# Performance work log

Hardware: AMD Instinct MI355X
Metric: run time of the kernel (lower is better)

## Reference

```python
import jax, jax.numpy as jnp
import numpy as np
import math

B, N, D, H = 2, 96, 64, 4  # batch, num_nodes, d_model, num_heads
DK = D // H


def setup_inputs() -> dict:
    key = jax.random.key(0)
    ks = jax.random.split(key, 11)
    s = 0.02
    return {
        "state": jax.random.normal(ks[0], (B, N * N, D), jnp.float32),
        "w_lk": jax.random.normal(ks[1], (D, D), jnp.float32) * s,
        "b_lk": jax.random.normal(ks[2], (D,), jnp.float32) * s,
        "w_rk": jax.random.normal(ks[3], (D, D), jnp.float32) * s,
        "b_rk": jax.random.normal(ks[4], (D,), jnp.float32) * s,
        "w_lv": jax.random.normal(ks[5], (D, D), jnp.float32) * s,
        "b_lv": jax.random.normal(ks[6], (D,), jnp.float32) * s,
        "w_rv": jax.random.normal(ks[7], (D, D), jnp.float32) * s,
        "b_rv": jax.random.normal(ks[8], (D,), jnp.float32) * s,
        "w_out": jax.random.normal(ks[9], (D, D), jnp.float32) * s,
        "b_out": jax.random.normal(ks[10], (D,), jnp.float32) * s,
    }


def reference(state, w_lk, b_lk, w_rk, b_rk, w_lv, b_lv, w_rv, b_rv, w_out, b_out):
    b = state.shape[0]
    n = int(np.sqrt(state.shape[1]))
    d_model = state.shape[2]
    h, dk = H, d_model // H

    def lin(x, w, bias):  # torch nn.Linear: x @ W^T + b
        return x @ w.T + bias

    # project and view as [b, n, n, h, dk]
    lk = lin(state, w_lk, b_lk).reshape(b, n, n, h, dk)
    rk = lin(state, w_rk, b_rk).reshape(b, n, n, h, dk)
    lv = lin(state, w_lv, b_lv).reshape(b, n, n, h, dk)
    rv = lin(state, w_rv, b_rv).reshape(b, n, n, h, dk)

    # triangular edge-attention scores over intermediate node a
    scores = jnp.einsum('bxahd,bayhd->bxayh', lk, rk) / math.sqrt(dk)
    att = jax.nn.softmax(scores, axis=2)  # softmax over a

    # fused contraction: equivalent to val = lv[x,a]*rv[a,y] then sum_a att*val,
    # without materializing the O(n^3 * d) val tensor
    x = jnp.einsum('bxayh,bxahd,bayhd->bxyhd', att, lv, rv)

    x = x.reshape(b, n * n, d_model)
    return lin(x, w_out, b_out)
```

## Files before the change

### kernel.cpp

```cpp
#include <hip/hip_runtime.h>

#define TENS   1179648
#define HM     147456
#define T_ROWS 18432
#define NP_S   6

__global__ __launch_bounds__(256) void proj4_kernel(
    const float* __restrict__ state,
    const float* __restrict__ w0, const float* __restrict__ b0,
    const float* __restrict__ w1, const float* __restrict__ b1,
    const float* __restrict__ w2, const float* __restrict__ b2,
    const float* __restrict__ w3, const float* __restrict__ b3,
    float* __restrict__ o0, float* __restrict__ o1,
    float* __restrict__ o2, float* __restrict__ o3)
{
    __shared__ float swt[64 * 68];
    __shared__ float srow[128 * 68];
    __shared__ float sb[64];
    const int t = threadIdx.x;
    const int mat = blockIdx.x & 3;
    const int g   = blockIdx.x >> 2;
    const int row0 = g * 128;
    const float* w  = (mat == 0) ? w0 : (mat == 1) ? w1 : (mat == 2) ? w2 : w3;
    const float* bi = (mat == 0) ? b0 : (mat == 1) ? b1 : (mat == 2) ? b2 : b3;
    float* o        = (mat == 0) ? o0 : (mat == 1) ? o1 : (mat == 2) ? o2 : o3;

#pragma unroll
    for (int j = 0; j < 4; ++j) {
        const int s = t + j * 256;
        const int c = s >> 4, k4 = s & 15;
        const float4 wv = *(const float4*)(w + c * 64 + k4 * 4);
        swt[(k4 * 4 + 0) * 68 + c] = wv.x;
        swt[(k4 * 4 + 1) * 68 + c] = wv.y;
        swt[(k4 * 4 + 2) * 68 + c] = wv.z;
        swt[(k4 * 4 + 3) * 68 + c] = wv.w;
    }
#pragma unroll
    for (int j = 0; j < 8; ++j) {
        const int s = t + j * 256;
        const int row = s >> 4, k4 = s & 15;
        *(float4*)&srow[row * 68 + k4 * 4] =
            *(const float4*)(state + (size_t)(row0 + row) * 64 + k4 * 4);
    }
    if (t < 64) sb[t] = bi[t];
    __syncthreads();

    const int c4 = t & 15, rg = t >> 4;
    const float4 binit = *(const float4*)&sb[c4 * 4];
    float4 acc[8];
#pragma unroll
    for (int rr = 0; rr < 8; ++rr) acc[rr] = binit;

#pragma unroll
    for (int k4 = 0; k4 < 16; ++k4) {
        const float4 wq0 = *(const float4*)&swt[(k4 * 4 + 0) * 68 + c4 * 4];
        const float4 wq1 = *(const float4*)&swt[(k4 * 4 + 1) * 68 + c4 * 4];
        const float4 wq2 = *(const float4*)&swt[(k4 * 4 + 2) * 68 + c4 * 4];
        const float4 wq3 = *(const float4*)&swt[(k4 * 4 + 3) * 68 + c4 * 4];
#pragma unroll
        for (int rr = 0; rr < 8; ++rr) {
            const float4 s4 = *(const float4*)&srow[(rg + rr * 16) * 68 + k4 * 4];
            acc[rr].x = fmaf(s4.x, wq0.x, acc[rr].x);
            acc[rr].y = fmaf(s4.x, wq0.y, acc[rr].y);
            acc[rr].z = fmaf(s4.x, wq0.z, acc[rr].z);
            acc[rr].w = fmaf(s4.x, wq0.w, acc[rr].w);
            acc[rr].x = fmaf(s4.y, wq1.x, acc[rr].x);
            acc[rr].y = fmaf(s4.y, wq1.y, acc[rr].y);
            acc[rr].z = fmaf(s4.y, wq1.z, acc[rr].z);
            acc[rr].w = fmaf(s4.y, wq1.w, acc[rr].w);
            acc[rr].x = fmaf(s4.z, wq2.x, acc[rr].x);
            acc[rr].y = fmaf(s4.z, wq2.y, acc[rr].y);
            acc[rr].z = fmaf(s4.z, wq2.z, acc[rr].z);
            acc[rr].w = fmaf(s4.z, wq2.w, acc[rr].w);
            acc[rr].x = fmaf(s4.w, wq3.x, acc[rr].x);
            acc[rr].y = fmaf(s4.w, wq3.y, acc[rr].y);
            acc[rr].z = fmaf(s4.w, wq3.z, acc[rr].z);
            acc[rr].w = fmaf(s4.w, wq3.w, acc[rr].w);
        }
    }
    const int b  = row0 / 9216;
    const int h  = c4 >> 2;
    const int dq = c4 & 3;
    float* dp = o + (size_t)(b * 4 + h) * HM + dq * 4;
    const int rb0 = row0 - b * 9216 + rg;
#pragma unroll
    for (int rr = 0; rr < 8; ++rr)
        *(float4*)(dp + (size_t)(rb0 + rr * 16) * 16) = acc[rr];
}

__global__ __launch_bounds__(256) void fused_attn_kernel(
    const float* __restrict__ lk, const float* __restrict__ rk,
    const float* __restrict__ lv, const float* __restrict__ rv,
    float* __restrict__ nump, float* __restrict__ denp)
{
    __shared__ float lk_s[2176];
    __shared__ float lv_s[2176];
    __shared__ float rk_s[2560];
    __shared__ float rv_s[2560];

    const int t = threadIdx.x;
    const int j = blockIdx.x;
    const int bh = j & 7;
    const int r2 = j >> 3;
    const int sc = r2 % 6;
    const int tile = r2 / 6;
    const int xt = tile % 3, yt = tile / 3;
    const int x0 = xt * 32, y0 = yt * 32;
    const int a00 = sc * 16;
    const int xi2 = t & 15, yi2 = t >> 4;

    const float* plk = lk + (size_t)bh * HM;
    const float* prk = rk + (size_t)bh * HM;
    const float* plv = lv + (size_t)bh * HM;
    const float* prv = rv + (size_t)bh * HM;

    float4 a00v = {0.f,0.f,0.f,0.f}, a01v = a00v, a02v = a00v, a03v = a00v;
    float4 a10v = a00v, a11v = a00v, a12v = a00v, a13v = a00v;
    float4 a20v = a00v, a21v = a00v, a22v = a00v, a23v = a00v;
    float4 a30v = a00v, a31v = a00v, a32v = a00v, a33v = a00v;
    float d00 = 0.f, d01 = 0.f, d10 = 0.f, d11 = 0.f;

    for (int acx = 0; acx < 4; ++acx) {
        const int a0 = a00 + acx * 4;
        __syncthreads();
#pragma unroll
        for (int jj = 0; jj < 2; ++jj) {
            const int slot = t + jj * 256;
            const int xl = slot >> 4, rem = slot & 15;
            const int ai = rem >> 2, c4 = rem & 3;
            const int goff = ((x0 + xl) * 96 + a0 + ai) * 16 + c4 * 4;
            const int loff = ((xl & 1) * 16 + (xl >> 1)) * 68 + ai * 16 + c4 * 4;
            *(float4*)&lk_s[loff] = *(const float4*)(plk + goff);
            *(float4*)&lv_s[loff] = *(const float4*)(plv + goff);
        }
#pragma unroll
        for (int jj = 0; jj < 2; ++jj) {
            const int slot = t + jj * 256;
            const int ai = slot >> 7, rem = slot & 127;
            const int yl = rem >> 2, c4 = rem & 3;
            const int goff = ((a0 + ai) * 96 + y0 + yl) * 16 + c4 * 4;
            const int loff = ai * 640 + ((yl & 1) * 16 + (yl >> 1)) * 20 + c4 * 4;
            *(float4*)&rk_s[loff] = *(const float4*)(prk + goff);
            *(float4*)&rv_s[loff] = *(const float4*)(prv + goff);
        }
        __syncthreads();
#pragma unroll
        for (int ai = 0; ai < 4; ++ai) {
            const int lo0 = xi2 * 68 + ai * 16;
            const int lo1 = (16 + xi2) * 68 + ai * 16;
            const int ro0 = ai * 640 + yi2 * 20;
            const int ro1 = ai * 640 + (16 + yi2) * 20;
            const float4 ka0 = *(const float4*)&lk_s[lo0];
            const float4 ka1 = *(const float4*)&lk_s[lo0 + 4];
            const float4 ka2 = *(const float4*)&lk_s[lo0 + 8];
            const float4 ka3 = *(const float4*)&lk_s[lo0 + 12];
            const float4 kb0 = *(const float4*)&lk_s[lo1];
            const float4 kb1 = *(const float4*)&lk_s[lo1 + 4];
            const float4 kb2 = *(const float4*)&lk_s[lo1 + 8];
            const float4 kb3 = *(const float4*)&lk_s[lo1 + 12];
            const float4 qa0 = *(const float4*)&rk_s[ro0];
            const float4 qa1 = *(const float4*)&rk_s[ro0 + 4];
            const float4 qa2 = *(const float4*)&rk_s[ro0 + 8];
            const float4 qa3 = *(const float4*)&rk_s[ro0 + 12];
            const float4 qb0 = *(const float4*)&rk_s[ro1];
            const float4 qb1 = *(const float4*)&rk_s[ro1 + 4];
            const float4 qb2 = *(const float4*)&rk_s[ro1 + 8];
            const float4 qb3 = *(const float4*)&rk_s[ro1 + 12];

#define DOT16(A0,A1,A2,A3,B0,B1,B2,B3)                                   \
    fmaf(A3.w,B3.w, fmaf(A3.z,B3.z, fmaf(A3.y,B3.y, fmaf(A3.x,B3.x,     \
    fmaf(A2.w,B2.w, fmaf(A2.z,B2.z, fmaf(A2.y,B2.y, fmaf(A2.x,B2.x,     \
    fmaf(A1.w,B1.w, fmaf(A1.z,B1.z, fmaf(A1.y,B1.y, fmaf(A1.x,B1.x,     \
    fmaf(A0.w,B0.w, fmaf(A0.z,B0.z, fmaf(A0.y,B0.y, A0.x*B0.x)))))))))))))))
            const float s00 = DOT16(ka0,ka1,ka2,ka3, qa0,qa1,qa2,qa3);
            const float s01 = DOT16(ka0,ka1,ka2,ka3, qb0,qb1,qb2,qb3);
            const float s10 = DOT16(kb0,kb1,kb2,kb3, qa0,qa1,qa2,qa3);
            const float s11 = DOT16(kb0,kb1,kb2,kb3, qb0,qb1,qb2,qb3);
#undef DOT16
            const float p00 = __expf(s00 * 0.25f);
            const float p01 = __expf(s01 * 0.25f);
            const float p10 = __expf(s10 * 0.25f);
            const float p11 = __expf(s11 * 0.25f);
            d00 += p00; d01 += p01; d10 += p10; d11 += p11;

            const float4 la0 = *(const float4*)&lv_s[lo0];
            const float4 la1 = *(const float4*)&lv_s[lo0 + 4];
            const float4 la2 = *(const float4*)&lv_s[lo0 + 8];
            const float4 la3 = *(const float4*)&lv_s[lo0 + 12];
            const float4 lb0 = *(const float4*)&lv_s[lo1];
            const float4 lb1 = *(const float4*)&lv_s[lo1 + 4];
            const float4 lb2 = *(const float4*)&lv_s[lo1 + 8];
            const float4 lb3 = *(const float4*)&lv_s[lo1 + 12];
            const float4 va0 = *(const float4*)&rv_s[ro0];
            const float4 va1 = *(const float4*)&rv_s[ro0 + 4];
            const float4 va2 = *(const float4*)&rv_s[ro0 + 8];
            const float4 va3 = *(const float4*)&rv_s[ro0 + 12];
            const float4 vb0 = *(const float4*)&rv_s[ro1];
            const float4 vb1 = *(const float4*)&rv_s[ro1 + 4];
            const float4 vb2 = *(const float4*)&rv_s[ro1 + 8];
            const float4 vb3 = *(const float4*)&rv_s[ro1 + 12];

#define ACC4(AC, P, L, V)                       \
    AC.x = fmaf(P * L.x, V.x, AC.x);            \
    AC.y = fmaf(P * L.y, V.y, AC.y);            \
    AC.z = fmaf(P * L.z, V.z, AC.z);            \
    AC.w = fmaf(P * L.w, V.w, AC.w);
            ACC4(a00v, p00, la0, va0) ACC4(a01v, p00, la1, va1)
            ACC4(a02v, p00, la2, va2) ACC4(a03v, p00, la3, va3)
            ACC4(a10v, p01, la0, vb0) ACC4(a11v, p01, la1, vb1)
            ACC4(a12v, p01, la2, vb2) ACC4(a13v, p01, la3, vb3)
            ACC4(a20v, p10, lb0, va0) ACC4(a21v, p10, lb1, va1)
            ACC4(a22v, p10, lb2, va2) ACC4(a23v, p10, lb3, va3)
            ACC4(a30v, p11, lb0, vb0) ACC4(a31v, p11, lb1, vb1)
            ACC4(a32v, p11, lb2, vb2) ACC4(a33v, p11, lb3, vb3)
#undef ACC4
        }
    }

    const size_t pb = (size_t)(sc * 8 + bh) * 9216;
    const int xA = x0 + 2 * xi2, yA = y0 + 2 * yi2;
    {
        const size_t rb = pb + (size_t)xA * 96 + yA;
        float4* np = (float4*)(nump + rb * 16);
        np[0] = a00v; np[1] = a01v; np[2] = a02v; np[3] = a03v;
        denp[rb] = d00;
    }
    {
        const size_t rb = pb + (size_t)xA * 96 + yA + 1;
        float4* np = (float4*)(nump + rb * 16);
        np[0] = a10v; np[1] = a11v; np[2] = a12v; np[3] = a13v;
        denp[rb] = d01;
    }
    {
        const size_t rb = pb + (size_t)(xA + 1) * 96 + yA;
        float4* np = (float4*)(nump + rb * 16);
        np[0] = a20v; np[1] = a21v; np[2] = a22v; np[3] = a23v;
        denp[rb] = d10;
    }
    {
        const size_t rb = pb + (size_t)(xA + 1) * 96 + yA + 1;
        float4* np = (float4*)(nump + rb * 16);
        np[0] = a30v; np[1] = a31v; np[2] = a32v; np[3] = a33v;
        denp[rb] = d11;
    }
}

__global__ __launch_bounds__(256) void proj1_kernel(
    const float* __restrict__ nump, const float* __restrict__ denp,
    const float* __restrict__ w, const float* __restrict__ bi,
    float* __restrict__ out)
{
    __shared__ float swt[64 * 68];
    __shared__ float srow[128 * 68];
    __shared__ float sb[64];
    const int t = threadIdx.x;
    const int row0 = blockIdx.x * 128;
    const int bb  = row0 / 9216;
    const int rb0 = row0 - bb * 9216;

#pragma unroll
    for (int j = 0; j < 4; ++j) {
        const int s = t + j * 256;
        const int c = s >> 4, k4 = s & 15;
        const float4 wv = *(const float4*)(w + c * 64 + k4 * 4);
        swt[(k4 * 4 + 0) * 68 + c] = wv.x;
        swt[(k4 * 4 + 1) * 68 + c] = wv.y;
        swt[(k4 * 4 + 2) * 68 + c] = wv.z;
        swt[(k4 * 4 + 3) * 68 + c] = wv.w;
    }
#pragma unroll
    for (int j = 0; j < 8; ++j) {
        const int s = t + j * 256;
        const int rl = s >> 4, hc = s & 15;
        const int bh = bb * 4 + (hc >> 2);
        const int c4g = hc & 3;
        const int rb = rb0 + rl;
        float sx = 0.f, sy = 0.f, sz = 0.f, sw4 = 0.f, dd = 0.f;
#pragma unroll
        for (int sc = 0; sc < NP_S; ++sc) {
            const size_t rbs = (size_t)(sc * 8 + bh) * 9216 + rb;
            const float4 v = *(const float4*)(nump + rbs * 16 + c4g * 4);
            sx += v.x; sy += v.y; sz += v.z; sw4 += v.w;
            dd += denp[rbs];
        }
        const float inv = 1.0f / dd;
        float4 ov; ov.x = sx * inv; ov.y = sy * inv; ov.z = sz * inv; ov.w = sw4 * inv;
        *(float4*)&srow[rl * 68 + hc * 4] = ov;
    }
    if (t < 64) sb[t] = bi[t];
    __syncthreads();

    const int c4 = t & 15, rg = t >> 4;
    const float4 binit = *(const float4*)&sb[c4 * 4];
    float4 acc[8];
#pragma unroll
    for (int rr = 0; rr < 8; ++rr) acc[rr] = binit;

#pragma unroll
    for (int k4 = 0; k4 < 16; ++k4) {
        const float4 wq0 = *(const float4*)&swt[(k4 * 4 + 0) * 68 + c4 * 4];
        const float4 wq1 = *(const float4*)&swt[(k4 * 4 + 1) * 68 + c4 * 4];
        const float4 wq2 = *(const float4*)&swt[(k4 * 4 + 2) * 68 + c4 * 4];
        const float4 wq3 = *(const float4*)&swt[(k4 * 4 + 3) * 68 + c4 * 4];
#pragma unroll
        for (int rr = 0; rr < 8; ++rr) {
            const float4 s4 = *(const float4*)&srow[(rg + rr * 16) * 68 + k4 * 4];
            acc[rr].x = fmaf(s4.x, wq0.x, acc[rr].x);
            acc[rr].y = fmaf(s4.x, wq0.y, acc[rr].y);
            acc[rr].z = fmaf(s4.x, wq0.z, acc[rr].z);
            acc[rr].w = fmaf(s4.x, wq0.w, acc[rr].w);
            acc[rr].x = fmaf(s4.y, wq1.x, acc[rr].x);
            acc[rr].y = fmaf(s4.y, wq1.y, acc[rr].y);
            acc[rr].z = fmaf(s4.y, wq1.z, acc[rr].z);
            acc[rr].w = fmaf(s4.y, wq1.w, acc[rr].w);
            acc[rr].x = fmaf(s4.z, wq2.x, acc[rr].x);
            acc[rr].y = fmaf(s4.z, wq2.y, acc[rr].y);
            acc[rr].z = fmaf(s4.z, wq2.z, acc[rr].z);
            acc[rr].w = fmaf(s4.z, wq2.w, acc[rr].w);
            acc[rr].x = fmaf(s4.w, wq3.x, acc[rr].x);
            acc[rr].y = fmaf(s4.w, wq3.y, acc[rr].y);
            acc[rr].z = fmaf(s4.w, wq3.z, acc[rr].z);
            acc[rr].w = fmaf(s4.w, wq3.w, acc[rr].w);
        }
    }
#pragma unroll
    for (int rr = 0; rr < 8; ++rr)
        *(float4*)(out + (size_t)(row0 + rg + rr * 16) * 64 + c4 * 4) = acc[rr];
}

extern "C" void kernel_launch(void* const* d_in, const int* in_sizes, int n_in,
                              void* d_out, int out_size, void* d_ws, size_t ws_size,
                              hipStream_t stream)
{
    const float* state = (const float*)d_in[0];
    const float* w_lk  = (const float*)d_in[1];
    const float* b_lk  = (const float*)d_in[2];
    const float* w_rk  = (const float*)d_in[3];
    const float* b_rk  = (const float*)d_in[4];
    const float* w_lv  = (const float*)d_in[5];
    const float* b_lv  = (const float*)d_in[6];
    const float* w_rv  = (const float*)d_in[7];
    const float* b_rv  = (const float*)d_in[8];
    const float* w_out = (const float*)d_in[9];
    const float* b_out = (const float*)d_in[10];
    float* out = (float*)d_out;

    float* ws = (float*)d_ws;
    float* lk   = ws;
    float* rk   = ws + (size_t)TENS;
    float* lv   = ws + (size_t)2 * TENS;
    float* rv   = ws + (size_t)3 * TENS;
    float* nump = ws + (size_t)4 * TENS;
    float* denp = nump + (size_t)NP_S * 8 * 9216 * 16;

    proj4_kernel<<<4 * (T_ROWS / 128), 256, 0, stream>>>(
        state, w_lk, b_lk, w_rk, b_rk, w_lv, b_lv, w_rv, b_rv, lk, rk, lv, rv);
    fused_attn_kernel<<<432, 256, 0, stream>>>(lk, rk, lv, rv, nump, denp);
    proj1_kernel<<<T_ROWS / 128, 256, 0, stream>>>(nump, denp, w_out, b_out, out);
}
```

Baseline: 137.2 us.

## Fuse three kernels into one persistent kernel with software grid barriers

Merges the projection, attention and output-projection kernels into a single 432-block kernel that separates the stages with atomic-counter grid barriers, and resets the counters with a memset before launch. The goal is to remove the launch gaps and tail effects between the three kernels. The projection stage now loops over jobs so 432 blocks cover 576 work items. The output stage uses only 144 of the blocks. The barrier assumes every block is resident at once, which launch_bounds(256,2) is meant to make possible, and the extra memset adds a small fixed cost.

```diff
diff --git a/kernel.cpp b/kernel.cpp
--- a/kernel.cpp
+++ b/kernel.cpp
@@ -4,328 +4,345 @@
 #define HM     147456
 #define T_ROWS 18432
 #define NP_S   6
-
-__global__ __launch_bounds__(256) void proj4_kernel(
+#define NBLK   432
+
+__device__ __forceinline__ void grid_barrier(unsigned* __restrict__ bar, int slot)
+{
+    __threadfence();
+    __syncthreads();
+    if (threadIdx.x == 0) {
+        atomicAdd(&bar[slot], 1u);
+        while (atomicAdd(&bar[slot], 0u) < (unsigned)NBLK) {
+            __builtin_amdgcn_s_sleep(2);
+        }
+    }
+    __syncthreads();
+    __threadfence();
+}
+
+__global__ __launch_bounds__(256, 2) void mega_kernel(
     const float* __restrict__ state,
     const float* __restrict__ w0, const float* __restrict__ b0,
     const float* __restrict__ w1, const float* __restrict__ b1,
     const float* __restrict__ w2, const float* __restrict__ b2,
     const float* __restrict__ w3, const float* __restrict__ b3,
-    float* __restrict__ o0, float* __restrict__ o1,
-    float* __restrict__ o2, float* __restrict__ o3)
+    const float* __restrict__ w4, const float* __restrict__ b4,
+    float* __restrict__ lk, float* __restrict__ rk,
+    float* __restrict__ lv, float* __restrict__ rv,
+    float* __restrict__ nump, float* __restrict__ denp,
+    unsigned* __restrict__ bar,
+    float* __restrict__ out)
 {
-    __shared__ float swt[64 * 68];
-    __shared__ float srow[128 * 68];
-    __shared__ float sb[64];
-    const int t = threadIdx.x;
-    const int mat = blockIdx.x & 3;
-    const int g   = blockIdx.x >> 2;
-    const int row0 = g * 128;
-    const float* w  = (mat == 0) ? w0 : (mat == 1) ? w1 : (mat == 2) ? w2 : w3;
-    const float* bi = (mat == 0) ? b0 : (mat == 1) ? b1 : (mat == 2) ? b2 : b3;
-    float* o        = (mat == 0) ? o0 : (mat == 1) ? o1 : (mat == 2) ? o2 : o3;
-
-#pragma unroll
-    for (int j = 0; j < 4; ++j) {
-        const int s = t + j * 256;
-        const int c = s >> 4, k4 = s & 15;
-        const float4 wv = *(const float4*)(w + c * 64 + k4 * 4);
-        swt[(k4 * 4 + 0) * 68 + c] = wv.x;
-        swt[(k4 * 4 + 1) * 68 + c] = wv.y;
-        swt[(k4 * 4 + 2) * 68 + c] = wv.z;
-        swt[(k4 * 4 + 3) * 68 + c] = wv.w;
+    __shared__ float smem[13120];
+    const int t   = threadIdx.x;
+    const int bid = blockIdx.x;
+
+    {
+        float* swt  = smem;
+        float* srow = smem + 4352;
+        float* sb   = smem + 13056;
+        for (int job = bid; job < 576; job += NBLK) {
+            const int mat = job & 3;
+            const int g   = job >> 2;
+            const int row0 = g * 128;
+            const float* w  = (mat == 0) ? w0 : (mat == 1) ? w1 : (mat == 2) ? w2 : w3;
+            const float* bi = (mat == 0) ? b0 : (mat == 1) ? b1 : (mat == 2) ? b2 : b3;
+            float* o        = (mat == 0) ? lk : (mat == 1) ? rk : (mat == 2) ? lv : rv;
+
+            __syncthreads();
+#pragma unroll
+            for (int j = 0; j < 4; ++j) {
+                const int s = t + j * 256;
+                const int c = s >> 4, k4 = s & 15;
+                const float4 wv = *(const float4*)(w + c * 64 + k4 * 4);
+                swt[(k4 * 4 + 0) * 68 + c] = wv.x;
+                swt[(k4 * 4 + 1) * 68 + c] = wv.y;
+                swt[(k4 * 4 + 2) * 68 + c] = wv.z;
+                swt[(k4 * 4 + 3) * 68 + c] = wv.w;
+            }
+#pragma unroll
+            for (int j = 0; j < 8; ++j) {
+                const int s = t + j * 256;
+                const int row = s >> 4, k4 = s & 15;
+                *(float4*)&srow[row * 68 + k4 * 4] =
+                    *(const float4*)(state + (size_t)(row0 + row) * 64 + k4 * 4);
+            }
+            if (t < 64) sb[t] = bi[t];
+            __syncthreads();
+
+            const int c4 = t & 15, rg = t >> 4;
+            const float4 binit = *(const float4*)&sb[c4 * 4];
+            float4 acc[8];
+#pragma unroll
+            for (int rr = 0; rr < 8; ++rr) acc[rr] = binit;
+#pragma unroll
+            for (int k4 = 0; k4 < 16; ++k4) {
+                const float4 wq0 = *(const float4*)&swt[(k4 * 4 + 0) * 68 + c4 * 4];
+                const float4 wq1 = *(const float4*)&swt[(k4 * 4 + 1) * 68 + c4 * 4];
+                const float4 wq2 = *(const float4*)&swt[(k4 * 4 + 2) * 68 + c4 * 4];
+                const float4 wq3 = *(const float4*)&swt[(k4 * 4 + 3) * 68 + c4 * 4];
+#pragma unroll
+                for (int rr = 0; rr < 8; ++rr) {
+                    const float4 s4 = *(const float4*)&srow[(rg + rr * 16) * 68 + k4 * 4];
+                    acc[rr].x = fmaf(s4.x, wq0.x, acc[rr].x);
+                    acc[rr].y = fmaf(s4.x, wq0.y, acc[rr].y);
+                    acc[rr].z = fmaf(s4.x, wq0.z, acc[rr].z);
+                    acc[rr].w = fmaf(s4.x, wq0.w, acc[rr].w);
+                    acc[rr].x = fmaf(s4.y, wq1.x, acc[rr].x);
+                    acc[rr].y = fmaf(s4.y, wq1.y, acc[rr].y);
+                    acc[rr].z = fmaf(s4.y, wq1.z, acc[rr].z);
+                    acc[rr].w = fmaf(s4.y, wq1.w, acc[rr].w);
+                    acc[rr].x = fmaf(s4.z, wq2.x, acc[rr].x);
+                    acc[rr].y = fmaf(s4.z, wq2.y, acc[rr].y);
+                    acc[rr].z = fmaf(s4.z, wq2.z, acc[rr].z);
+                    acc[rr].w = fmaf(s4.z, wq2.w, acc[rr].w);
+                    acc[rr].x = fmaf(s4.w, wq3.x, acc[rr].x);
+                    acc[rr].y = fmaf(s4.w, wq3.y, acc[rr].y);
+                    acc[rr].z = fmaf(s4.w, wq3.z, acc[rr].z);
+                    acc[rr].w = fmaf(s4.w, wq3.w, acc[rr].w);
+                }
+            }
+            const int b  = row0 / 9216;
+            const int h  = c4 >> 2;
+            const int dq = c4 & 3;
+            float* dp = o + (size_t)(b * 4 + h) * HM + dq * 4;
+            const int rb0 = row0 - b * 9216 + rg;
+#pragma unroll
+            for (int rr = 0; rr < 8; ++rr)
+                *(float4*)(dp + (size_t)(rb0 + rr * 16) * 16) = acc[rr];
+        }
     }
-#pragma unroll
-    for (int j = 0; j < 8; ++j) {
-        const int s = t + j * 256;
-        const int row = s >> 4, k4 = s & 15;
-        *(float4*)&srow[row * 68 + k4 * 4] =
-            *(const float4*)(state + (size_t)(row0 + row) * 64 + k4 * 4);
-    }
-    if (t < 64) sb[t] = bi[t];
-    __syncthreads();
-
-    const int c4 = t & 15, rg = t >> 4;
-    const float4 binit = *(const float4*)&sb[c4 * 4];
-    float4 acc[8];
-#pragma unroll
-    for (int rr = 0; rr < 8; ++rr) acc[rr] = binit;
-
-#pragma unroll
-    for (int k4 = 0; k4 < 16; ++k4) {
-        const float4 wq0 = *(const float4*)&swt[(k4 * 4 + 0) * 68 + c4 * 4];
-        const float4 wq1 = *(const float4*)&swt[(k4 * 4 + 1) * 68 + c4 * 4];
-        const float4 wq2 = *(const float4*)&swt[(k4 * 4 + 2) * 68 + c4 * 4];
-        const float4 wq3 = *(const float4*)&swt[(k4 * 4 + 3) * 68 + c4 * 4];
-#pragma unroll
-        for (int rr = 0; rr < 8; ++rr) {
-            const float4 s4 = *(const float4*)&srow[(rg + rr * 16) * 68 + k4 * 4];
-            acc[rr].x = fmaf(s4.x, wq0.x, acc[rr].x);
-            acc[rr].y = fmaf(s4.x, wq0.y, acc[rr].y);
-            acc[rr].z = fmaf(s4.x, wq0.z, acc[rr].z);
-            acc[rr].w = fmaf(s4.x, wq0.w, acc[rr].w);
-            acc[rr].x = fmaf(s4.y, wq1.x, acc[rr].x);
-            acc[rr].y = fmaf(s4.y, wq1.y, acc[rr].y);
-            acc[rr].z = fmaf(s4.y, wq1.z, acc[rr].z);
-            acc[rr].w = fmaf(s4.y, wq1.w, acc[rr].w);
-            acc[rr].x = fmaf(s4.z, wq2.x, acc[rr].x);
-            acc[rr].y = fmaf(s4.z, wq2.y, acc[rr].y);
-            acc[rr].z = fmaf(s4.z, wq2.z, acc[rr].z);
-            acc[rr].w = fmaf(s4.z, wq2.w, acc[rr].w);
-            acc[rr].x = fmaf(s4.w, wq3.x, acc[rr].x);
-            acc[rr].y = fmaf(s4.w, wq3.y, acc[rr].y);
-            acc[rr].z = fmaf(s4.w, wq3.z, acc[rr].z);
-            acc[rr].w = fmaf(s4.w, wq3.w, acc[rr].w);
-        }
-    }
-    const int b  = row0 / 9216;
-    const int h  = c4 >> 2;
-    const int dq = c4 & 3;
-    float* dp = o + (size_t)(b * 4 + h) * HM + dq * 4;
-    const int rb0 = row0 - b * 9216 + rg;
-#pragma unroll
-    for (int rr = 0; rr < 8; ++rr)
-        *(float4*)(dp + (size_t)(rb0 + rr * 16) * 16) = acc[rr];
-}
-
-__global__ __launch_bounds__(256) void fused_attn_kernel(
-    const float* __restrict__ lk, const float* __restrict__ rk,
-    const float* __restrict__ lv, const float* __restrict__ rv,
-    float* __restrict__ nump, float* __restrict__ denp)
-{
-    __shared__ float lk_s[2176];
-    __shared__ float lv_s[2176];
-    __shared__ float rk_s[2560];
-    __shared__ float rv_s[2560];
-
-    const int t = threadIdx.x;
-    const int j = blockIdx.x;
-    const int bh = j & 7;
-    const int r2 = j >> 3;
-    const int sc = r2 % 6;
-    const int tile = r2 / 6;
-    const int xt = tile % 3, yt = tile / 3;
-    const int x0 = xt * 32, y0 = yt * 32;
-    const int a00 = sc * 16;
-    const int xi2 = t & 15, yi2 = t >> 4;
-
-    const float* plk = lk + (size_t)bh * HM;
-    const float* prk = rk + (size_t)bh * HM;
-    const float* plv = lv + (size_t)bh * HM;
-    const float* prv = rv + (size_t)bh * HM;
-
-    float4 a00v = {0.f,0.f,0.f,0.f}, a01v = a00v, a02v = a00v, a03v = a00v;
-    float4 a10v = a00v, a11v = a00v, a12v = a00v, a13v = a00v;
-    float4 a20v = a00v, a21v = a00v, a22v = a00v, a23v = a00v;
-    float4 a30v = a00v, a31v = a00v, a32v = a00v, a33v = a00v;
-    float d00 = 0.f, d01 = 0.f, d10 = 0.f, d11 = 0.f;
-
-    for (int acx = 0; acx < 4; ++acx) {
-        const int a0 = a00 + acx * 4;
-        __syncthreads();
-#pragma unroll
-        for (int jj = 0; jj < 2; ++jj) {
-            const int slot = t + jj * 256;
-            const int xl = slot >> 4, rem = slot & 15;
-            const int ai = rem >> 2, c4 = rem & 3;
-            const int goff = ((x0 + xl) * 96 + a0 + ai) * 16 + c4 * 4;
-            const int loff = ((xl & 1) * 16 + (xl >> 1)) * 68 + ai * 16 + c4 * 4;
-            *(float4*)&lk_s[loff] = *(const float4*)(plk + goff);
-            *(float4*)&lv_s[loff] = *(const float4*)(plv + goff);
-        }
-#pragma unroll
-        for (int jj = 0; jj < 2; ++jj) {
-            const int slot = t + jj * 256;
-            const int ai = slot >> 7, rem = slot & 127;
-            const int yl = rem >> 2, c4 = rem & 3;
-            const int goff = ((a0 + ai) * 96 + y0 + yl) * 16 + c4 * 4;
-            const int loff = ai * 640 + ((yl & 1) * 16 + (yl >> 1)) * 20 + c4 * 4;
-            *(float4*)&rk_s[loff] = *(const float4*)(prk + goff);
-            *(float4*)&rv_s[loff] = *(const float4*)(prv + goff);
-        }
-        __syncthreads();
-#pragma unroll
-        for (int ai = 0; ai < 4; ++ai) {
-            const int lo0 = xi2 * 68 + ai * 16;
-            const int lo1 = (16 + xi2) * 68 + ai * 16;
-            const int ro0 = ai * 640 + yi2 * 20;
-            const int ro1 = ai * 640 + (16 + yi2) * 20;
-            const float4 ka0 = *(const float4*)&lk_s[lo0];
-            const float4 ka1 = *(const float4*)&lk_s[lo0 + 4];
-            const float4 ka2 = *(const float4*)&lk_s[lo0 + 8];
-            const float4 ka3 = *(const float4*)&lk_s[lo0 + 12];
-            const float4 kb0 = *(const float4*)&lk_s[lo1];
-            const float4 kb1 = *(const float4*)&lk_s[lo1 + 4];
-            const float4 kb2 = *(const float4*)&lk_s[lo1 + 8];
-            const float4 kb3 = *(const float4*)&lk_s[lo1 + 12];
-            const float4 qa0 = *(const float4*)&rk_s[ro0];
-            const float4 qa1 = *(const float4*)&rk_s[ro0 + 4];
-            const float4 qa2 = *(const float4*)&rk_s[ro0 + 8];
-            const float4 qa3 = *(const float4*)&rk_s[ro0 + 12];
-            const float4 qb0 = *(const float4*)&rk_s[ro1];
-            const float4 qb1 = *(const float4*)&rk_s[ro1 + 4];
-            const float4 qb2 = *(const float4*)&rk_s[ro1 + 8];
-            const float4 qb3 = *(const float4*)&rk_s[ro1 + 12];
+    grid_barrier(bar, 0);
+
+    {
+        float* lk_s = smem;
+        float* lv_s = smem + 2176;
+        float* rk_s = smem + 4352;
+        float* rv_s = smem + 6912;
+        const int jb = bid;
+        const int bh = jb & 7;
+        const int r2 = jb >> 3;
+        const int sc = r2 % 6;
+        const int tile = r2 / 6;
+        const int xt = tile % 3, yt = tile / 3;
+        const int x0 = xt * 32, y0 = yt * 32;
+        const int a00 = sc * 16;
+        const int xi2 = t & 15, yi2 = t >> 4;
+
+        const float* plk = lk + (size_t)bh * HM;
+        const float* prk = rk + (size_t)bh * HM;
+        const float* plv = lv + (size_t)bh * HM;
+        const float* prv = rv + (size_t)bh * HM;
+
+        float4 a00v = {0.f,0.f,0.f,0.f}, a01v = a00v, a02v = a00v, a03v = a00v;
+        float4 a10v = a00v, a11v = a00v, a12v = a00v, a13v = a00v;
+        float4 a20v = a00v, a21v = a00v, a22v = a00v, a23v = a00v;
+        float4 a30v = a00v, a31v = a00v, a32v = a00v, a33v = a00v;
+        float d00 = 0.f, d01 = 0.f, d10 = 0.f, d11 = 0.f;
+
+        for (int acx = 0; acx < 4; ++acx) {
+            const int a0 = a00 + acx * 4;
+            __syncthreads();
+#pragma unroll
+            for (int jj = 0; jj < 2; ++jj) {
+                const int slot = t + jj * 256;
+                const int xl = slot >> 4, rem = slot & 15;
+                const int ai = rem >> 2, c4 = rem & 3;
+                const int goff = ((x0 + xl) * 96 + a0 + ai) * 16 + c4 * 4;
+                const int loff = ((xl & 1) * 16 + (xl >> 1)) * 68 + ai * 16 + c4 * 4;
+                *(float4*)&lk_s[loff] = *(const float4*)(plk + goff);
+                *(float4*)&lv_s[loff] = *(const float4*)(plv + goff);
+            }
+#pragma unroll
+            for (int jj = 0; jj < 2; ++jj) {
+                const int slot = t + jj * 256;
+                const int ai = slot >> 7, rem = slot & 127;
+                const int yl = rem >> 2, c4 = rem & 3;
+                const int goff = ((a0 + ai) * 96 + y0 + yl) * 16 + c4 * 4;
+                const int loff = ai * 640 + ((yl & 1) * 16 + (yl >> 1)) * 20 + c4 * 4;
+                *(float4*)&rk_s[loff] = *(const float4*)(prk + goff);
+                *(float4*)&rv_s[loff] = *(const float4*)(prv + goff);
+            }
+            __syncthreads();
+#pragma unroll
+            for (int ai = 0; ai < 4; ++ai) {
+                const int lo0 = xi2 * 68 + ai * 16;
+                const int lo1 = (16 + xi2) * 68 + ai * 16;
+                const int ro0 = ai * 640 + yi2 * 20;
+                const int ro1 = ai * 640 + (16 + yi2) * 20;
+                const float4 ka0 = *(const float4*)&lk_s[lo0];
+                const float4 ka1 = *(const float4*)&lk_s[lo0 + 4];
+                const float4 ka2 = *(const float4*)&lk_s[lo0 + 8];
+                const float4 ka3 = *(const float4*)&lk_s[lo0 + 12];
+                const float4 kb0 = *(const float4*)&lk_s[lo1];
+                const float4 kb1 = *(const float4*)&lk_s[lo1 + 4];
+                const float4 kb2 = *(const float4*)&lk_s[lo1 + 8];
+                const float4 kb3 = *(const float4*)&lk_s[lo1 + 12];
+                const float4 qa0 = *(const float4*)&rk_s[ro0];
+                const float4 qa1 = *(const float4*)&rk_s[ro0 + 4];
+                const float4 qa2 = *(const float4*)&rk_s[ro0 + 8];
+                const float4 qa3 = *(const float4*)&rk_s[ro0 + 12];
+                const float4 qb0 = *(const float4*)&rk_s[ro1];
+                const float4 qb1 = *(const float4*)&rk_s[ro1 + 4];
+                const float4 qb2 = *(const float4*)&rk_s[ro1 + 8];
+                const float4 qb3 = *(const float4*)&rk_s[ro1 + 12];
 
 #define DOT16(A0,A1,A2,A3,B0,B1,B2,B3)                                   \
     fmaf(A3.w,B3.w, fmaf(A3.z,B3.z, fmaf(A3.y,B3.y, fmaf(A3.x,B3.x,     \
     fmaf(A2.w,B2.w, fmaf(A2.z,B2.z, fmaf(A2.y,B2.y, fmaf(A2.x,B2.x,     \
     fmaf(A1.w,B1.w, fmaf(A1.z,B1.z, fmaf(A1.y,B1.y, fmaf(A1.x,B1.x,     \
     fmaf(A0.w,B0.w, fmaf(A0.z,B0.z, fmaf(A0.y,B0.y, A0.x*B0.x)))))))))))))))
-            const float s00 = DOT16(ka0,ka1,ka2,ka3, qa0,qa1,qa2,qa3);
-            const float s01 = DOT16(ka0,ka1,ka2,ka3, qb0,qb1,qb2,qb3);
-            const float s10 = DOT16(kb0,kb1,kb2,kb3, qa0,qa1,qa2,qa3);
-            const float s11 = DOT16(kb0,kb1,kb2,kb3, qb0,qb1,qb2,qb3);
+                const float s00 = DOT16(ka0,ka1,ka2,ka3, qa0,qa1,qa2,qa3);
+                const float s01 = DOT16(ka0,ka1,ka2,ka3, qb0,qb1,qb2,qb3);
+                const float s10 = DOT16(kb0,kb1,kb2,kb3, qa0,qa1,qa2,qa3);
+                const float s11 = DOT16(kb0,kb1,kb2,kb3, qb0,qb1,qb2,qb3);
 #undef DOT16
-            const float p00 = __expf(s00 * 0.25f);
-            const float p01 = __expf(s01 * 0.25f);
-            const float p10 = __expf(s10 * 0.25f);
-            const float p11 = __expf(s11 * 0.25f);
-            d00 += p00; d01 += p01; d10 += p10; d11 += p11;
-
-            const float4 la0 = *(const float4*)&lv_s[lo0];
-            const float4 la1 = *(const float4*)&lv_s[lo0 + 4];
-            const float4 la2 = *(const float4*)&lv_s[lo0 + 8];
-            const float4 la3 = *(const float4*)&lv_s[lo0 + 12];
-            const float4 lb0 = *(const float4*)&lv_s[lo1];
-            const float4 lb1 = *(const float4*)&lv_s[lo1 + 4];
-            const float4 lb2 = *(const float4*)&lv_s[lo1 + 8];
-            const float4 lb3 = *(const float4*)&lv_s[lo1 + 12];
-            const float4 va0 = *(const float4*)&rv_s[ro0];
-            const float4 va1 = *(const float4*)&rv_s[ro0 + 4];
-            const float4 va2 = *(const float4*)&rv_s[ro0 + 8];
-            const float4 va3 = *(const float4*)&rv_s[ro0 + 12];
-            const float4 vb0 = *(const float4*)&rv_s[ro1];
-            const float4 vb1 = *(const float4*)&rv_s[ro1 + 4];
-            const float4 vb2 = *(const float4*)&rv_s[ro1 + 8];
-            const float4 vb3 = *(const float4*)&rv_s[ro1 + 12];
+                const float p00 = __expf(s00 * 0.25f);
+                const float p01 = __expf(s01 * 0.25f);
+                const float p10 = __expf(s10 * 0.25f);
+                const float p11 = __expf(s11 * 0.25f);
+                d00 += p00; d01 += p01; d10 += p10; d11 += p11;
+
+                const float4 la0 = *(const float4*)&lv_s[lo0];
+                const float4 la1 = *(const float4*)&lv_s[lo0 + 4];
+                const float4 la2 = *(const float4*)&lv_s[lo0 + 8];
+                const float4 la3 = *(const float4*)&lv_s[lo0 + 12];
+                const float4 lb0 = *(const float4*)&lv_s[lo1];
+                const float4 lb1 = *(const float4*)&lv_s[lo1 + 4];
+                const float4 lb2 = *(const float4*)&lv_s[lo1 + 8];
+                const float4 lb3 = *(const float4*)&lv_s[lo1 + 12];
+                const float4 va0 = *(const float4*)&rv_s[ro0];
+                const float4 va1 = *(const float4*)&rv_s[ro0 + 4];
+                const float4 va2 = *(const float4*)&rv_s[ro0 + 8];
+                const float4 va3 = *(const float4*)&rv_s[ro0 + 12];
+                const float4 vb0 = *(const float4*)&rv_s[ro1];
+                const float4 vb1 = *(const float4*)&rv_s[ro1 + 4];
+                const float4 vb2 = *(const float4*)&rv_s[ro1 + 8];
+                const float4 vb3 = *(const float4*)&rv_s[ro1 + 12];
 
 #define ACC4(AC, P, L, V)                       \
     AC.x = fmaf(P * L.x, V.x, AC.x);            \
     AC.y = fmaf(P * L.y, V.y, AC.y);            \
     AC.z = fmaf(P * L.z, V.z, AC.z);            \
     AC.w = fmaf(P * L.w, V.w, AC.w);
-            ACC4(a00v, p00, la0, va0) ACC4(a01v, p00, la1, va1)
-            ACC4(a02v, p00, la2, va2) ACC4(a03v, p00, la3, va3)
-            ACC4(a10v, p01, la0, vb0) ACC4(a11v, p01, la1, vb1)
-            ACC4(a12v, p01, la2, vb2) ACC4(a13v, p01, la3, vb3)
-            ACC4(a20v, p10, lb0, va0) ACC4(a21v, p10, lb1, va1)
-            ACC4(a22v, p10, lb2, va2) ACC4(a23v, p10, lb3, va3)
-            ACC4(a30v, p11, lb0, vb0) ACC4(a31v, p11, lb1, vb1)
-            ACC4(a32v, p11, lb2, vb2) ACC4(a33v, p11, lb3, vb3)
+                ACC4(a00v, p00, la0, va0) ACC4(a01v, p00, la1, va1)
+                ACC4(a02v, p00, la2, va2) ACC4(a03v, p00, la3, va3)
+                ACC4(a10v, p01, la0, vb0) ACC4(a11v, p01, la1, vb1)
+                ACC4(a12v, p01, la2, vb2) ACC4(a13v, p01, la3, vb3)
+                ACC4(a20v, p10, lb0, va0) ACC4(a21v, p10, lb1, va1)
+                ACC4(a22v, p10, lb2, va2) ACC4(a23v, p10, lb3, va3)
+                ACC4(a30v, p11, lb0, vb0) ACC4(a31v, p11, lb1, vb1)
+                ACC4(a32v, p11, lb2, vb2) ACC4(a33v, p11, lb3, vb3)
 #undef ACC4
+            }
+        }
+
+        const size_t pb = (size_t)(sc * 8 + bh) * 9216;
+        const int xA = x0 + 2 * xi2, yA = y0 + 2 * yi2;
+        {
+            const size_t rb = pb + (size_t)xA * 96 + yA;
+            float4* np = (float4*)(nump + rb * 16);
+            np[0] = a00v; np[1] = a01v; np[2] = a02v; np[3] = a03v;
+            denp[rb] = d00;
+        }
+        {
+            const size_t rb = pb + (size_t)xA * 96 + yA + 1;
+            float4* np = (float4*)(nump + rb * 16);
+            np[0] = a10v; np[1] = a11v; np[2] = a12v; np[3] = a13v;
+            denp[rb] = d01;
+        }
+        {
+            const size_t rb = pb + (size_t)(xA + 1) * 96 + yA;
+            float4* np = (float4*)(nump + rb * 16);
+            np[0] = a20v; np[1] = a21v; np[2] = a22v; np[3] = a23v;
+            denp[rb] = d10;
+        }
+        {
+            const size_t rb = pb + (size_t)(xA + 1) * 96 + yA + 1;
+            float4* np = (float4*)(nump + rb * 16);
+            np[0] = a30v; np[1] = a31v; np[2] = a32v; np[3] = a33v;
+            denp[rb] = d11;
         }
     }
-
-    const size_t pb = (size_t)(sc * 8 + bh) * 9216;
-    const int xA = x0 + 2 * xi2, yA = y0 + 2 * yi2;
-    {
-        const size_t rb = pb + (size_t)xA * 96 + yA;
-        float4* np = (float4*)(nump + rb * 16);
-        np[0] = a00v; np[1] = a01v; np[2] = a02v; np[3] = a03v;
-        denp[rb] = d00;
+    grid_barrier(bar, 1);
+
+    if (bid < 144) {
+        float* swt  = smem;
+        float* srow = smem + 4352;
+        float* sb   = smem + 13056;
+        const int row0 = bid * 128;
+        const int bb  = row0 / 9216;
+        const int rb0 = row0 - bb * 9216;
+
+        __syncthreads();
+#pragma unroll
+        for (int j = 0; j < 4; ++j) {
+            const int s = t + j * 256;
+            const int c = s >> 4, k4 = s & 15;
+            const float4 wv = *(const float4*)(w4 + c * 64 + k4 * 4);
+            swt[(k4 * 4 + 0) * 68 + c] = wv.x;
+            swt[(k4 * 4 + 1) * 68 + c] = wv.y;
+            swt[(k4 * 4 + 2) * 68 + c] = wv.z;
+            swt[(k4 * 4 + 3) * 68 + c] = wv.w;
+        }
+#pragma unroll
+        for (int j = 0; j < 8; ++j) {
+            const int s = t + j * 256;
+            const int rl = s >> 4, hc = s & 15;
+            const int bh = bb * 4 + (hc >> 2);
+            const int c4g = hc & 3;
+            const int rb = rb0 + rl;
+            float sx = 0.f, sy = 0.f, sz = 0.f, sw4 = 0.f, dd = 0.f;
+#pragma unroll
+            for (int sc = 0; sc < NP_S; ++sc) {
+                const size_t rbs = (size_t)(sc * 8 + bh) * 9216 + rb;
+                const float4 v = *(const float4*)(nump + rbs * 16 + c4g * 4);
+                sx += v.x; sy += v.y; sz += v.z; sw4 += v.w;
+                dd += denp[rbs];
+            }
+            const float inv = 1.0f / dd;
+            float4 ov; ov.x = sx * inv; ov.y = sy * inv; ov.z = sz * inv; ov.w = sw4 * inv;
+            *(float4*)&srow[rl * 68 + hc * 4] = ov;
+        }
+        if (t < 64) sb[t] = b4[t];
+        __syncthreads();
+
+        const int c4 = t & 15, rg = t >> 4;
+        const float4 binit = *(const float4*)&sb[c4 * 4];
+        float4 acc[8];
+#pragma unroll
+        for (int rr = 0; rr < 8; ++rr) acc[rr] = binit;
+#pragma unroll
+        for (int k4 = 0; k4 < 16; ++k4) {
+            const float4 wq0 = *(const float4*)&swt[(k4 * 4 + 0) * 68 + c4 * 4];
+            const float4 wq1 = *(const float4*)&swt[(k4 * 4 + 1) * 68 + c4 * 4];
+            const float4 wq2 = *(const float4*)&swt[(k4 * 4 + 2) * 68 + c4 * 4];
+            const float4 wq3 = *(const float4*)&swt[(k4 * 4 + 3) * 68 + c4 * 4];
+#pragma unroll
+            for (int rr = 0; rr < 8; ++rr) {
+                const float4 s4 = *(const float4*)&srow[(rg + rr * 16) * 68 + k4 * 4];
+                acc[rr].x = fmaf(s4.x, wq0.x, acc[rr].x);
+                acc[rr].y = fmaf(s4.x, wq0.y, acc[rr].y);
+                acc[rr].z = fmaf(s4.x, wq0.z, acc[rr].z);
+                acc[rr].w = fmaf(s4.x, wq0.w, acc[rr].w);
+                acc[rr].x = fmaf(s4.y, wq1.x, acc[rr].x);
+                acc[rr].y = fmaf(s4.y, wq1.y, acc[rr].y);
+                acc[rr].z = fmaf(s4.y, wq1.z, acc[rr].z);
+                acc[rr].w = fmaf(s4.y, wq1.w, acc[rr].w);
+                acc[rr].x = fmaf(s4.z, wq2.x, acc[rr].x);
+                acc[rr].y = fmaf(s4.z, wq2.y, acc[rr].y);
+                acc[rr].z = fmaf(s4.z, wq2.z, acc[rr].z);
+                acc[rr].w = fmaf(s4.z, wq2.w, acc[rr].w);
+                acc[rr].x = fmaf(s4.w, wq3.x, acc[rr].x);
+                acc[rr].y = fmaf(s4.w, wq3.y, acc[rr].y);
+                acc[rr].z = fmaf(s4.w, wq3.z, acc[rr].z);
+                acc[rr].w = fmaf(s4.w, wq3.w, acc[rr].w);
+            }
+        }
+#pragma unroll
+        for (int rr = 0; rr < 8; ++rr)
+            *(float4*)(out + (size_t)(row0 + rg + rr * 16) * 64 + c4 * 4) = acc[rr];
     }
-    {
-        const size_t rb = pb + (size_t)xA * 96 + yA + 1;
-        float4* np = (float4*)(nump + rb * 16);
-        np[0] = a10v; np[1] = a11v; np[2] = a12v; np[3] = a13v;
-        denp[rb] = d01;
-    }
-    {
-        const size_t rb = pb + (size_t)(xA + 1) * 96 + yA;
-        float4* np = (float4*)(nump + rb * 16);
-        np[0] = a20v; np[1] = a21v; np[2] = a22v; np[3] = a23v;
-        denp[rb] = d10;
-    }
-    {
-        const size_t rb = pb + (size_t)(xA + 1) * 96 + yA + 1;
-        float4* np = (float4*)(nump + rb * 16);
-        np[0] = a30v; np[1] = a31v; np[2] = a32v; np[3] = a33v;
-        denp[rb] = d11;
-    }
-}
-
-__global__ __launch_bounds__(256) void proj1_kernel(
-    const float* __restrict__ nump, const float* __restrict__ denp,
-    const float* __restrict__ w, const float* __restrict__ bi,
-    float* __restrict__ out)
-{
-    __shared__ float swt[64 * 68];
-    __shared__ float srow[128 * 68];
-    __shared__ float sb[64];
-    const int t = threadIdx.x;
-    const int row0 = blockIdx.x * 128;
-    const int bb  = row0 / 9216;
-    const int rb0 = row0 - bb * 9216;
-
-#pragma unroll
-    for (int j = 0; j < 4; ++j) {
-        const int s = t + j * 256;
-        const int c = s >> 4, k4 = s & 15;
-        const float4 wv = *(const float4*)(w + c * 64 + k4 * 4);
-        swt[(k4 * 4 + 0) * 68 + c] = wv.x;
-        swt[(k4 * 4 + 1) * 68 + c] = wv.y;
-        swt[(k4 * 4 + 2) * 68 + c] = wv.z;
-        swt[(k4 * 4 + 3) * 68 + c] = wv.w;
-    }
-#pragma unroll
-    for (int j = 0; j < 8; ++j) {
-        const int s = t + j * 256;
-        const int rl = s >> 4, hc = s & 15;
-        const int bh = bb * 4 + (hc >> 2);
-        const int c4g = hc & 3;
-        const int rb = rb0 + rl;
-        float sx = 0.f, sy = 0.f, sz = 0.f, sw4 = 0.f, dd = 0.f;
-#pragma unroll
-        for (int sc = 0; sc < NP_S; ++sc) {
-            const size_t rbs = (size_t)(sc * 8 + bh) * 9216 + rb;
-            const float4 v = *(const float4*)(nump + rbs * 16 + c4g * 4);
-            sx += v.x; sy += v.y; sz += v.z; sw4 += v.w;
-            dd += denp[rbs];
-        }
-        const float inv = 1.0f / dd;
-        float4 ov; ov.x = sx * inv; ov.y = sy * inv; ov.z = sz * inv; ov.w = sw4 * inv;
-        *(float4*)&srow[rl * 68 + hc * 4] = ov;
-    }
-    if (t < 64) sb[t] = bi[t];
-    __syncthreads();
-
-    const int c4 = t & 15, rg = t >> 4;
-    const float4 binit = *(const float4*)&sb[c4 * 4];
-    float4 acc[8];
-#pragma unroll
-    for (int rr = 0; rr < 8; ++rr) acc[rr] = binit;
-
-#pragma unroll
-    for (int k4 = 0; k4 < 16; ++k4) {
-        const float4 wq0 = *(const float4*)&swt[(k4 * 4 + 0) * 68 + c4 * 4];
-        const float4 wq1 = *(const float4*)&swt[(k4 * 4 + 1) * 68 + c4 * 4];
-        const float4 wq2 = *(const float4*)&swt[(k4 * 4 + 2) * 68 + c4 * 4];
-        const float4 wq3 = *(const float4*)&swt[(k4 * 4 + 3) * 68 + c4 * 4];
-#pragma unroll
-        for (int rr = 0; rr < 8; ++rr) {
-            const float4 s4 = *(const float4*)&srow[(rg + rr * 16) * 68 + k4 * 4];
-            acc[rr].x = fmaf(s4.x, wq0.x, acc[rr].x);
-            acc[rr].y = fmaf(s4.x, wq0.y, acc[rr].y);
-            acc[rr].z = fmaf(s4.x, wq0.z, acc[rr].z);
-            acc[rr].w = fmaf(s4.x, wq0.w, acc[rr].w);
-            acc[rr].x = fmaf(s4.y, wq1.x, acc[rr].x);
-            acc[rr].y = fmaf(s4.y, wq1.y, acc[rr].y);
-            acc[rr].z = fmaf(s4.y, wq1.z, acc[rr].z);
-            acc[rr].w = fmaf(s4.y, wq1.w, acc[rr].w);
-            acc[rr].x = fmaf(s4.z, wq2.x, acc[rr].x);
-            acc[rr].y = fmaf(s4.z, wq2.y, acc[rr].y);
-            acc[rr].z = fmaf(s4.z, wq2.z, acc[rr].z);
-            acc[rr].w = fmaf(s4.z, wq2.w, acc[rr].w);
-            acc[rr].x = fmaf(s4.w, wq3.x, acc[rr].x);
-            acc[rr].y = fmaf(s4.w, wq3.y, acc[rr].y);
-            acc[rr].z = fmaf(s4.w, wq3.z, acc[rr].z);
-            acc[rr].w = fmaf(s4.w, wq3.w, acc[rr].w);
-        }
-    }
-#pragma unroll
-    for (int rr = 0; rr < 8; ++rr)
-        *(float4*)(out + (size_t)(row0 + rg + rr * 16) * 64 + c4 * 4) = acc[rr];
 }
 
 extern "C" void kernel_launch(void* const* d_in, const int* in_sizes, int n_in,
@@ -352,9 +369,10 @@
     float* rv   = ws + (size_t)3 * TENS;
     float* nump = ws + (size_t)4 * TENS;
     float* denp = nump + (size_t)NP_S * 8 * 9216 * 16;
-
-    proj4_kernel<<<4 * (T_ROWS / 128), 256, 0, stream>>>(
-        state, w_lk, b_lk, w_rk, b_rk, w_lv, b_lv, w_rv, b_rv, lk, rk, lv, rv);
-    fused_attn_kernel<<<432, 256, 0, stream>>>(lk, rk, lv, rv, nump, denp);
-    proj1_kernel<<<T_ROWS / 128, 256, 0, stream>>>(nump, denp, w_out, b_out, out);
+    unsigned* bar = (unsigned*)(denp + (size_t)NP_S * 8 * 9216);
+
+    hipMemsetAsync(bar, 0, 2 * sizeof(unsigned), stream);
+    mega_kernel<<<NBLK, 256, 0, stream>>>(
+        state, w_lk, b_lk, w_rk, b_rk, w_lv, b_lv, w_rv, b_rv, w_out, b_out,
+        lk, rk, lv, rv, nump, denp, bar, out);
 }
```

After: 368.9 us. 169% more time.
